# Optimization experiments

Measured on AMD Instinct MI355X. Metric: run time of the kernel, lower is better.

## Reference

```python
import jax, jax.numpy as jnp
import numpy as np

LN_EPS = 1e-5


def setup_inputs() -> dict:
    key = jax.random.key(0)
    k1, k2, k3 = jax.random.split(key, 3)
    N, E, D_IN, D_OUT = 50000, 500000, 128, 128
    x = jax.random.normal(k1, (N, D_IN), dtype=jnp.float32)
    edge_index = jax.random.randint(k2, (2, E), 0, N, dtype=jnp.int64)
    W = jax.random.normal(k3, (D_IN, D_OUT), dtype=jnp.float32) * (1.0 / np.sqrt(D_IN))
    b = jnp.zeros((D_OUT,), dtype=jnp.float32)
    ln_gamma = jnp.ones((D_OUT,), dtype=jnp.float32)
    ln_beta = jnp.zeros((D_OUT,), dtype=jnp.float32)
    return {"x": x, "edge_index": edge_index, "W": W, "b": b,
            "ln_gamma": ln_gamma, "ln_beta": ln_beta}


def reference(x, edge_index, W, b, ln_gamma, ln_beta):
    N = x.shape[0]
    # GCNConv: linear transform first (no fused bias; bias added after aggregation)
    h = x @ W  # [N, D_out]
    # add self-loops
    loops = jnp.arange(N, dtype=edge_index.dtype)
    src = jnp.concatenate([edge_index[0], loops])  # [E+N]
    dst = jnp.concatenate([edge_index[1], loops])  # [E+N]
    # symmetric normalization deg^{-1/2} (degree computed on dst, incl. self-loops)
    deg = jax.ops.segment_sum(jnp.ones(src.shape, dtype=h.dtype), dst, num_segments=N)
    dinv = jnp.where(deg > 0, jax.lax.rsqrt(deg), 0.0)
    norm = dinv[src] * dinv[dst]  # [E+N]
    # gather messages, scale, scatter-add to destinations
    msgs = h[src] * norm[:, None]  # [E+N, D_out]
    out = jax.ops.segment_sum(msgs, dst, num_segments=N) + b  # [N, D_out]
    # LayerNorm over features
    mu = out.mean(axis=-1, keepdims=True)
    var = out.var(axis=-1, keepdims=True)
    out = (out - mu) * jax.lax.rsqrt(var + LN_EPS) * ln_gamma + ln_beta
    # activation
    return jax.nn.relu(out)
```

## Files before the change

### kernel.cpp

```cpp
#include <hip/hip_runtime.h>
#include <hip/hip_fp16.h>
#include <math.h>

#define D 128
#define LN_EPS 1e-5f
#define BKT 64

typedef _Float16 f16x8 __attribute__((ext_vector_type(8)));
typedef float    f32x4 __attribute__((ext_vector_type(4)));

__global__ void prep_kernel(const float* __restrict__ W, _Float16* __restrict__ wtg,
                            int* __restrict__ degi, int N) {
    int idx = blockIdx.x * 256 + threadIdx.x;
    int k = idx >> 7;
    int n = idx & 127;
    wtg[n * D + k] = (_Float16)W[k * D + n];
    for (int i = idx; i < N; i += 64 * 256) degi[i] = 0;
}

__global__ void gemm_kernel(const float* __restrict__ x, const _Float16* __restrict__ wtg,
                            unsigned* __restrict__ h2, int N) {
    __shared__ _Float16 xs[64][136];
    int tid  = threadIdx.x;
    int row0 = blockIdx.x * 64;

#pragma unroll
    for (int i = 0; i < 8; ++i) {
        int idx = i * 256 + tid;
        int r   = idx >> 5;
        int c4  = idx & 31;
        float4 v = make_float4(0.f, 0.f, 0.f, 0.f);
        if (row0 + r < N) v = *(const float4*)&x[(size_t)(row0 + r) * D + c4 * 4];
        __half2 lo = __floats2half2_rn(v.x, v.y);
        __half2 hi = __floats2half2_rn(v.z, v.w);
        *(__half2*)&xs[r][c4 * 4]     = lo;
        *(__half2*)&xs[r][c4 * 4 + 2] = hi;
    }
    __syncthreads();

    int l     = tid & 63;
    int mtile = tid >> 6;
    int mn    = l & 15;
    int kq    = (l >> 4) * 8;
    f32x4 acc[8];
#pragma unroll
    for (int nt = 0; nt < 8; ++nt) acc[nt] = (f32x4){0.f, 0.f, 0.f, 0.f};

#pragma unroll
    for (int ks = 0; ks < 4; ++ks) {
        int kb = ks * 32 + kq;
        f16x8 a = *(f16x8*)&xs[mtile * 16 + mn][kb];
#pragma unroll
        for (int nt = 0; nt < 8; ++nt) {
            f16x8 bf = *(const f16x8*)&wtg[(nt * 16 + mn) * D + kb];
            acc[nt] = __builtin_amdgcn_mfma_f32_16x16x32_f16(a, bf, acc[nt], 0, 0, 0);
        }
    }

    int quad = l >> 4;
#pragma unroll
    for (int nt = 0; nt < 8; ++nt) {
#pragma unroll
        for (int rg = 0; rg < 4; ++rg) {
            float v  = acc[nt][rg];
            float pv = __shfl_xor(v, 1);
            if (!(l & 1)) {
                int row = row0 + mtile * 16 + quad * 4 + rg;
                if (row < N) {
                    __half2 p = __floats2half2_rn(v, pv);
                    h2[(size_t)row * (D / 2) + nt * 8 + (mn >> 1)] = *(unsigned*)&p;
                }
            }
        }
    }
}

__global__ void bucket_kernel(const int* __restrict__ src, const int* __restrict__ dst,
                              int* __restrict__ degi, int* __restrict__ bucket, int E) {
    int e = blockIdx.x * blockDim.x + threadIdx.x;
    if (e < E) {
        int d = dst[e];
        int p = atomicAdd(&degi[d], 1);
        if (p < BKT) bucket[(size_t)d * BKT + p] = src[e];
    }
}

__device__ __forceinline__ void acc_edge(float& a0, float& a1, unsigned u, float w) {
    __half2 hv = *(__half2*)&u;
    a0 = fmaf(__low2float(hv),  w, a0);
    a1 = fmaf(__high2float(hv), w, a1);
}

__global__ void gather_ln_kernel(const int* __restrict__ bucket, const int* __restrict__ degi,
                                 const unsigned* __restrict__ h2, const float* __restrict__ b,
                                 const float* __restrict__ g, const float* __restrict__ be,
                                 float* __restrict__ out, int N) {
    int row  = blockIdx.x * 4 + (threadIdx.x >> 6);
    int lane = threadIdx.x & 63;
    if (row >= N) return;
    int dg   = degi[row];
    int dgc  = dg < BKT ? dg : BKT;
    float di = rsqrtf((float)dg + 1.0f);
    float sw = di * di;
    unsigned su = h2[(size_t)row * (D / 2) + lane];
    float acc0 = 0.f, acc1 = 0.f;
    acc_edge(acc0, acc1, su, sw);
    const int* bk = bucket + (size_t)row * BKT;
    int e = 0;
    for (; e + 7 < dgc; e += 8) {
        int s[8]; float wgt[8]; unsigned u[8];
#pragma unroll
        for (int j = 0; j < 8; ++j) s[j] = bk[e + j];
#pragma unroll
        for (int j = 0; j < 8; ++j) wgt[j] = rsqrtf((float)degi[s[j]] + 1.0f) * di;
#pragma unroll
        for (int j = 0; j < 8; ++j) u[j] = h2[(size_t)s[j] * (D / 2) + lane];
#pragma unroll
        for (int j = 0; j < 8; ++j) acc_edge(acc0, acc1, u[j], wgt[j]);
    }
    for (; e < dgc; ++e) {
        int s = bk[e];
        acc_edge(acc0, acc1, h2[(size_t)s * (D / 2) + lane],
                 rsqrtf((float)degi[s] + 1.0f) * di);
    }
    float2 bb = *(const float2*)&b[lane * 2];
    float v0 = acc0 + bb.x;
    float v1 = acc1 + bb.y;
    float s = v0 + v1;
    float q = v0 * v0 + v1 * v1;
#pragma unroll
    for (int off = 32; off; off >>= 1) {
        s += __shfl_xor(s, off);
        q += __shfl_xor(q, off);
    }
    float mean = s * (1.0f / 128.0f);
    float var  = q * (1.0f / 128.0f) - mean * mean;
    float rstd = rsqrtf(var + LN_EPS);
    float2 gg = *(const float2*)&g[lane * 2];
    float2 eb = *(const float2*)&be[lane * 2];
    float y0 = (v0 - mean) * rstd * gg.x + eb.x;
    float y1 = (v1 - mean) * rstd * gg.y + eb.y;
    *(float2*)&out[(size_t)row * D + lane * 2] = make_float2(fmaxf(y0, 0.0f), fmaxf(y1, 0.0f));
}

extern "C" void kernel_launch(void* const* d_in, const int* in_sizes, int n_in,
                              void* d_out, int out_size, void* d_ws, size_t ws_size,
                              hipStream_t stream) {
    const float* x  = (const float*)d_in[0];
    const int*   ei = (const int*)d_in[1];
    const float* W  = (const float*)d_in[2];
    const float* b  = (const float*)d_in[3];
    const float* g  = (const float*)d_in[4];
    const float* be = (const float*)d_in[5];

    int N = in_sizes[0] / D;
    int E = in_sizes[1] / 2;
    const int* src = ei;
    const int* dst = ei + E;

    float* out = (float*)d_out;

    char* w = (char*)d_ws;
    unsigned* h2    = (unsigned*)w;           w += (size_t)N * (D / 2) * sizeof(unsigned);
    int*      degi  = (int*)w;                w += (size_t)N * sizeof(int);
    _Float16* wtg   = (_Float16*)w;           w += (size_t)D * D * sizeof(_Float16);
    int*      bucket= (int*)w;                w += (size_t)N * BKT * sizeof(int);

    prep_kernel   <<<64,               256, 0, stream>>>(W, wtg, degi, N);
    gemm_kernel   <<<(N + 63) / 64,    256, 0, stream>>>(x, wtg, h2, N);
    bucket_kernel <<<(E + 255) / 256,  256, 0, stream>>>(src, dst, degi, bucket, E);
    gather_ln_kernel<<<(N + 3) / 4,    256, 0, stream>>>(bucket, degi, h2,
                                                         b, g, be, out, N);
}
```

Baseline: 167.8 us.

## Fuse GEMM and edge bucketing into one launch; vectorize bucket reads in gather

Merges the GEMM and the edge-bucketing kernels into one grid, with block ranges split by role, so the two independent stages can run concurrently and one launch is dropped. The gather loop now reads bucket indices with int4 loads and handles the tail by masking rather than through a scalar remainder loop. Masked lanes point at the row itself and use zero weight, so they still issue redundant h2 loads. Bucket blocks also allocate the GEMM's shared memory, which can lower their occupancy.

```diff
diff --git a/kernel.cpp b/kernel.cpp
--- a/kernel.cpp
+++ b/kernel.cpp
@@ -18,12 +18,25 @@
     for (int i = idx; i < N; i += 64 * 256) degi[i] = 0;
 }
 
-__global__ void gemm_kernel(const float* __restrict__ x, const _Float16* __restrict__ wtg,
-                            unsigned* __restrict__ h2, int N) {
+__global__ void fused_kernel(const float* __restrict__ x, const _Float16* __restrict__ wtg,
+                             unsigned* __restrict__ h2,
+                             const int* __restrict__ src, const int* __restrict__ dst,
+                             int* __restrict__ degi, int* __restrict__ bucket,
+                             int N, int E, int nbG) {
     __shared__ _Float16 xs[64][136];
-    int tid  = threadIdx.x;
+    int tid = threadIdx.x;
+
+    if ((int)blockIdx.x >= nbG) {
+        int e = (blockIdx.x - nbG) * 256 + tid;
+        if (e < E) {
+            int d = dst[e];
+            int p = atomicAdd(&degi[d], 1);
+            if (p < BKT) bucket[(size_t)d * BKT + p] = src[e];
+        }
+        return;
+    }
+
     int row0 = blockIdx.x * 64;
-
 #pragma unroll
     for (int i = 0; i < 8; ++i) {
         int idx = i * 256 + tid;
@@ -75,16 +88,6 @@
     }
 }
 
-__global__ void bucket_kernel(const int* __restrict__ src, const int* __restrict__ dst,
-                              int* __restrict__ degi, int* __restrict__ bucket, int E) {
-    int e = blockIdx.x * blockDim.x + threadIdx.x;
-    if (e < E) {
-        int d = dst[e];
-        int p = atomicAdd(&degi[d], 1);
-        if (p < BKT) bucket[(size_t)d * BKT + p] = src[e];
-    }
-}
-
 __device__ __forceinline__ void acc_edge(float& a0, float& a1, unsigned u, float w) {
     __half2 hv = *(__half2*)&u;
     a0 = fmaf(__low2float(hv),  w, a0);
@@ -106,23 +109,25 @@
     float acc0 = 0.f, acc1 = 0.f;
     acc_edge(acc0, acc1, su, sw);
     const int* bk = bucket + (size_t)row * BKT;
-    int e = 0;
-    for (; e + 7 < dgc; e += 8) {
-        int s[8]; float wgt[8]; unsigned u[8];
+
+    for (int e = 0; e < dgc; e += 8) {
+        int4 ra = *(const int4*)&bk[e];
+        int4 rb = *(const int4*)&bk[e + 4];
+        int s[8];
+        s[0] = ra.x; s[1] = ra.y; s[2] = ra.z; s[3] = ra.w;
+        s[4] = rb.x; s[5] = rb.y; s[6] = rb.z; s[7] = rb.w;
+        float wgt[8]; unsigned u[8];
 #pragma unroll
-        for (int j = 0; j < 8; ++j) s[j] = bk[e + j];
-#pragma unroll
-        for (int j = 0; j < 8; ++j) wgt[j] = rsqrtf((float)degi[s[j]] + 1.0f) * di;
-#pragma unroll
-        for (int j = 0; j < 8; ++j) u[j] = h2[(size_t)s[j] * (D / 2) + lane];
+        for (int j = 0; j < 8; ++j) {
+            bool valid = (e + j) < dgc;
+            s[j] = valid ? s[j] : row;
+            u[j] = h2[(size_t)s[j] * (D / 2) + lane];
+            wgt[j] = valid ? rsqrtf((float)degi[s[j]] + 1.0f) * di : 0.0f;
+        }
 #pragma unroll
         for (int j = 0; j < 8; ++j) acc_edge(acc0, acc1, u[j], wgt[j]);
     }
-    for (; e < dgc; ++e) {
-        int s = bk[e];
-        acc_edge(acc0, acc1, h2[(size_t)s * (D / 2) + lane],
-                 rsqrtf((float)degi[s] + 1.0f) * di);
-    }
+
     float2 bb = *(const float2*)&b[lane * 2];
     float v0 = acc0 + bb.x;
     float v1 = acc1 + bb.y;
@@ -166,9 +171,12 @@
     _Float16* wtg   = (_Float16*)w;           w += (size_t)D * D * sizeof(_Float16);
     int*      bucket= (int*)w;                w += (size_t)N * BKT * sizeof(int);
 
-    prep_kernel   <<<64,               256, 0, stream>>>(W, wtg, degi, N);
-    gemm_kernel   <<<(N + 63) / 64,    256, 0, stream>>>(x, wtg, h2, N);
-    bucket_kernel <<<(E + 255) / 256,  256, 0, stream>>>(src, dst, degi, bucket, E);
-    gather_ln_kernel<<<(N + 3) / 4,    256, 0, stream>>>(bucket, degi, h2,
-                                                         b, g, be, out, N);
+    int nbG = (N + 63) / 64;
+    int nbB = (E + 255) / 256;
+
+    prep_kernel <<<64,        256, 0, stream>>>(W, wtg, degi, N);
+    fused_kernel<<<nbG + nbB, 256, 0, stream>>>(x, wtg, h2, src, dst, degi, bucket,
+                                                N, E, nbG);
+    gather_ln_kernel<<<(N + 3) / 4, 256, 0, stream>>>(bucket, degi, h2,
+                                                      b, g, be, out, N);
 }
```

Result: no change. 166.5 us (-0.8%).
